# Kernel optimization log

Measured on AMD Instinct MI355X. Metric: run time of the kernel, lower is better.

Reference implementation:

```python
import jax, jax.numpy as jnp
import numpy as np

N = 50000          # total nodes
NPG = 100          # nodes per graph
G = N // NPG       # graphs
E_RAND = 800000    # random intra-graph edges (no self loops)
F_IN, HID, OUT, H, NCLS = 128, 64, 64, 2, 10
NEG_SLOPE = 0.2


def setup_inputs() -> dict:
    key = jax.random.key(0)
    ks = jax.random.split(key, 16)
    x = jax.random.normal(ks[0], (N, F_IN), dtype=jnp.float32)
    # intra-graph edges, guaranteed non-self; PyG GATConv then appends self loops
    g = jax.random.randint(ks[1], (E_RAND,), 0, G)
    dst_loc = jax.random.randint(ks[2], (E_RAND,), 0, NPG)
    off = jax.random.randint(ks[3], (E_RAND,), 1, NPG)  # 1..NPG-1 -> never self
    src_loc = (dst_loc + off) % NPG
    base = g * NPG
    src = jnp.concatenate([base + src_loc, jnp.arange(N)])  # + self loops
    dst = jnp.concatenate([base + dst_loc, jnp.arange(N)])
    edge_index = jnp.stack([src, dst]).astype(jnp.int64)
    batch = (jnp.arange(N) // NPG).astype(jnp.int64)  # sorted segment ids
    y = jax.random.randint(ks[4], (N,), 0, NCLS).astype(jnp.int64)
    s = 0.1
    params = dict(
        W1=jax.random.normal(ks[5], (F_IN, H * HID), jnp.float32) * s,
        a_src1=jax.random.normal(ks[6], (H, HID), jnp.float32) * s,
        a_dst1=jax.random.normal(ks[7], (H, HID), jnp.float32) * s,
        b1=jnp.zeros((HID,), jnp.float32),
        W2=jax.random.normal(ks[8], (HID, H * OUT), jnp.float32) * s,
        a_src2=jax.random.normal(ks[9], (H, OUT), jnp.float32) * s,
        a_dst2=jax.random.normal(ks[10], (H, OUT), jnp.float32) * s,
        b2=jnp.zeros((OUT,), jnp.float32),
        Wc=jax.random.normal(ks[11], (OUT, NCLS), jnp.float32) * s,
        bc=jnp.zeros((NCLS,), jnp.float32),
    )
    return dict(x=x, edge_index=edge_index, batch=batch, y=y, **params)


def gat_layer(x, W, a_src, a_dst, b, src, dst, n_nodes):
    # PyG GATConv, heads=H, concat=False: h = xW -> [N,H,C]
    h = (x @ W).reshape(n_nodes, a_src.shape[0], a_src.shape[1])
    al_s = jnp.sum(h * a_src[None], axis=-1)  # [N,H]
    al_d = jnp.sum(h * a_dst[None], axis=-1)  # [N,H]
    e = jax.nn.leaky_relu(al_s[src] + al_d[dst], NEG_SLOPE)  # [E,H]
    # segment softmax over incoming edges of each dst node
    m = jax.ops.segment_max(e, dst, num_segments=n_nodes)  # every node has a self loop
    p = jnp.exp(e - m[dst])
    z = jax.ops.segment_sum(p, dst, num_segments=n_nodes)
    alpha = p / z[dst]  # [E,H]
    out = jax.ops.segment_sum(alpha[:, :, None] * h[src], dst, num_segments=n_nodes)
    return out.mean(axis=1) + b  # concat=False -> head mean, then bias


def reference(x, edge_index, batch, y, W1, a_src1, a_dst1, b1,
              W2, a_src2, a_dst2, b2, Wc, bc):
    # Per-graph loop in the original is equivalent to one pass over the batched
    # graph: edges are intra-graph and batch is sorted, so concatenation of
    # per-graph outputs preserves node order.
    src, dst = edge_index[0], edge_index[1]
    n = x.shape[0]
    h = gat_layer(x, W1, a_src1, a_dst1, b1, src, dst, n)
    h = jax.nn.relu(h)
    h = gat_layer(h, W2, a_src2, a_dst2, b2, src, dst, n)
    preds = h @ Wc + bc  # [N, num_classes]
    return preds, y
```

## Files before the change

### kernel.cpp

```cpp
#include <hip/hip_runtime.h>
#include <math.h>


#define NPG 100
#define CAP 2560
#define EPB 4096

#define OFF_HT    0
#define OFF_R3    34816
#define OFF_SCNT  65280
#define OFF_SAS   71680
#define OFF_SAD   72704
#define OFF_SRZ   73728
#define OFF_SWC   74176
#define OFF_SBC   76736
#define SMEM_BYTES 76800

typedef __attribute__((ext_vector_type(8))) short bf16x8;
typedef __attribute__((ext_vector_type(4))) float f32x4;

__device__ __forceinline__ float lrelu(float x) { return x > 0.f ? x : 0.2f * x; }

__device__ __forceinline__ unsigned cvt_pk(float lo, float hi) {
    unsigned r;
    asm("v_cvt_pk_bf16_f32 %0, %1, %2" : "=v"(r) : "v"(lo), "v"(hi));
    return r;
}

__device__ __forceinline__ unsigned short f2bf(float f) {
    unsigned int u = __float_as_uint(f);
    return (unsigned short)((u + 0x7FFF + ((u >> 16) & 1)) >> 16);
}

__global__ __launch_bounds__(1024) void bucket2_kernel(const int* __restrict__ src,
                                                       const int* __restrict__ dst,
                                                       int* gcnt,
                                                       unsigned short* __restrict__ bucket,
                                                       int e) {
    __shared__ int hist[512];
    __shared__ int base[512];
    __shared__ unsigned int staged[EPB];
    int tid = threadIdx.x;
    int e0 = blockIdx.x * EPB;
    int cnt = min(EPB, e - e0);

    for (int i = tid; i < 512; i += 1024) hist[i] = 0;
    __syncthreads();

    for (int i = tid; i < cnt; i += 1024) {
        int d = dst[e0 + i];
        int s = src[e0 + i];
        int g = d / NPG;
        int dloc = d - g * NPG;
        int sloc = s - g * NPG;
        staged[i] = ((unsigned)g << 16) | ((unsigned)dloc << 8) | (unsigned)sloc;
        atomicAdd(&hist[g], 1);
    }
    __syncthreads();

    if (tid < 512) {
        int h = hist[tid];
        base[tid] = h ? atomicAdd(&gcnt[tid], h) : 0;
        hist[tid] = 0;
    }
    __syncthreads();

    for (int i = tid; i < cnt; i += 1024) {
        unsigned v = staged[i];
        int g = v >> 16;
        int pos = base[g] + atomicAdd(&hist[g], 1);
        if (pos < CAP)
            bucket[(size_t)g * CAP + pos] = (unsigned short)(v & 0xFFFFu);
    }
}

__global__ __launch_bounds__(256) void convert_w(const float* __restrict__ W1,
                                                 const float* __restrict__ W2,
                                                 unsigned short* __restrict__ W1T,
                                                 unsigned short* __restrict__ W2T,
                                                 int* gcnt, int G) {
    int stride = gridDim.x * 256;
    int t0 = blockIdx.x * 256 + threadIdx.x;
    for (int i = t0; i < 128 * 128; i += stride) {
        int k = i >> 7, c = i & 127;
        W1T[c * 128 + k] = f2bf(W1[i]);
    }
    for (int i = t0; i < 64 * 128; i += stride) {
        int k = i >> 7, c = i & 127;
        W2T[c * 64 + k] = f2bf(W2[i]);
    }
    for (int i = t0; i < G; i += stride) gcnt[i] = 0;
}

template <int K, int SA>
__device__ __forceinline__ void gemm_block(const unsigned short* sA,
                                           const unsigned short* __restrict__ WT,
                                           const float* __restrict__ a_src,
                                           const float* __restrict__ a_dst,
                                           unsigned short* sHT,
                                           float* sAs, float* sAd,
                                           int lane, int wave) {
    if (wave >= 14) return;
    int s = wave >> 1, h = wave & 1;
    int fr = lane & 15, fk = (lane >> 4) * 8;
    f32x4 acc[4];
#pragma unroll
    for (int t = 0; t < 4; ++t) acc[t] = (f32x4){0.f, 0.f, 0.f, 0.f};
#pragma unroll
    for (int ks = 0; ks < K / 32; ++ks) {
        bf16x8 a = *reinterpret_cast<const bf16x8*>(&sA[(s * 16 + fr) * SA + ks * 32 + fk]);
#pragma unroll
        for (int t = 0; t < 4; ++t) {
            bf16x8 b = *reinterpret_cast<const bf16x8*>(
                &WT[((h * 4 + t) * 16 + fr) * K + ks * 32 + fk]);
            acc[t] = __builtin_amdgcn_mfma_f32_16x16x32_bf16(a, b, acc[t], 0, 0, 0);
        }
    }
    int rb = s * 16 + (lane >> 4) * 4;
    float ps[4] = {0, 0, 0, 0}, pd[4] = {0, 0, 0, 0};
#pragma unroll
    for (int t = 0; t < 4; ++t) {
        int col = (h * 4 + t) * 16 + fr;
        float as_ = a_src[col], ad_ = a_dst[col];
        float v0 = acc[t][0], v1 = acc[t][1], v2 = acc[t][2], v3 = acc[t][3];
        ps[0] += v0 * as_; pd[0] += v0 * ad_;
        ps[1] += v1 * as_; pd[1] += v1 * ad_;
        ps[2] += v2 * as_; pd[2] += v2 * ad_;
        ps[3] += v3 * as_; pd[3] += v3 * ad_;
        *reinterpret_cast<uint2*>(&sHT[col * 136 + rb]) =
            make_uint2(cvt_pk(v0, v1), cvt_pk(v2, v3));
    }
#pragma unroll
    for (int off = 1; off <= 8; off <<= 1) {
#pragma unroll
        for (int j = 0; j < 4; ++j) {
            ps[j] += __shfl_xor(ps[j], off);
            pd[j] += __shfl_xor(pd[j], off);
        }
    }
    if (fr == 0) {
#pragma unroll
        for (int j = 0; j < 4; ++j) {
            int d = rb + j;
            sAs[d * 2 + h] = ps[j];
            sAd[d * 2 + h] = pd[j];
        }
    }
}

__device__ __forceinline__ void agg_heads(unsigned short* sP,
                                          const unsigned short* sHT,
                                          const unsigned* scnt,
                                          const float* sAs, const float* sAd,
                                          float* sRZ, f32x4 res[2],
                                          int lane, int wave) {
    for (int head = 0; head < 2; ++head) {
        for (int d = wave; d < NPG; d += 16) {
            float adh = sAd[d * 2 + head];
            unsigned w = scnt[d * 16 + (lane >> 2)];
            int sh = (lane & 3) * 8;
            unsigned m0 = (w >> sh) & 15u;
            unsigned m1 = (w >> (sh + 4)) & 15u;
            float4 a4 = *reinterpret_cast<const float4*>(&sAs[lane * 4]);
            float e0 = (head ? a4.y : a4.x) + adh;
            float e1 = (head ? a4.w : a4.z) + adh;
            float p0 = m0 ? (float)m0 * __expf(lrelu(e0)) : 0.f;
            float p1 = m1 ? (float)m1 * __expf(lrelu(e1)) : 0.f;
            float z = p0 + p1;
            for (int off = 32; off; off >>= 1) z += __shfl_xor(z, off);
            *reinterpret_cast<unsigned*>(&sP[d * 136 + lane * 2]) = cvt_pk(p0, p1);
            if (lane == 0) sRZ[d] = 1.f / z;
        }
        __syncthreads();
#pragma unroll
        for (int i = 0; i < 2; ++i) {
            int t = wave + 16 * i;
            if (t < 28) {
                int mt = t >> 2, nt = t & 3;
                int arow = mt * 16 + (lane & 15);
                int brow = head * 64 + nt * 16 + (lane & 15);
                int kofs = (lane >> 4) * 8;
                f32x4 acc = (f32x4){0.f, 0.f, 0.f, 0.f};
#pragma unroll
                for (int ks = 0; ks < 4; ++ks) {
                    bf16x8 a = *reinterpret_cast<const bf16x8*>(&sP[arow * 136 + ks * 32 + kofs]);
                    bf16x8 b = *reinterpret_cast<const bf16x8*>(&sHT[brow * 136 + ks * 32 + kofs]);
                    acc = __builtin_amdgcn_mfma_f32_16x16x32_bf16(a, b, acc, 0, 0, 0);
                }
                int dbase = mt * 16 + (lane >> 4) * 4;
#pragma unroll
                for (int r = 0; r < 4; ++r)
                    res[i][r] += acc[r] * sRZ[dbase + r];
            }
        }
        __syncthreads();
    }
}

__global__ __launch_bounds__(1024, 8) void graph_fused(
    const float* __restrict__ x,
    const unsigned short* __restrict__ W1T,
    const unsigned short* __restrict__ W2T,
    const float* __restrict__ as1, const float* __restrict__ ad1,
    const float* __restrict__ b1,
    const float* __restrict__ as2, const float* __restrict__ ad2,
    const float* __restrict__ b2,
    const float* __restrict__ Wc, const float* __restrict__ bc,
    const int* __restrict__ gcnt, const unsigned short* __restrict__ bucket,
    const int* __restrict__ y,
    float* __restrict__ preds, float* __restrict__ yout) {
    extern __shared__ char smem[];
    unsigned short* sHT  = (unsigned short*)(smem + OFF_HT);
    float*          sOut = (float*)(smem + OFF_HT);
    unsigned short* R3u  = (unsigned short*)(smem + OFF_R3);
    unsigned*       scnt = (unsigned*)(smem + OFF_SCNT);
    float*          sAs  = (float*)(smem + OFF_SAS);
    float*          sAd  = (float*)(smem + OFF_SAD);
    float*          sRZ  = (float*)(smem + OFF_SRZ);
    float*          sWc  = (float*)(smem + OFF_SWC);
    float*          sbc  = (float*)(smem + OFF_SBC);

    int g = blockIdx.x, gbase = g * NPG, tid = threadIdx.x;
    int lane = tid & 63, wave = tid >> 6;
    int cnt = min(gcnt[g], CAP);
    float4 z4 = make_float4(0.f, 0.f, 0.f, 0.f);

    for (int i = tid; i < 1600; i += 1024) scnt[i] = 0;
    for (int i = tid; i < 2176; i += 1024)
        *reinterpret_cast<float4*>((char*)sHT + i * 16) = z4;
    for (int i = tid; i < NPG * 16; i += 1024) {
        int r = i >> 4, kc = (i & 15) * 8;
        const float* xp = &x[(size_t)(gbase + r) * 128 + kc];
        float4 v0 = *reinterpret_cast<const float4*>(xp);
        float4 v1 = *reinterpret_cast<const float4*>(xp + 4);
        uint4 u = make_uint4(cvt_pk(v0.x, v0.y), cvt_pk(v0.z, v0.w),
                             cvt_pk(v1.x, v1.y), cvt_pk(v1.z, v1.w));
        *reinterpret_cast<uint4*>(&R3u[r * 136 + kc]) = u;
    }
    for (int i = tid; i < 12 * 17; i += 1024) {
        int r = 100 + i / 17, c = (i % 17) * 8;
        *reinterpret_cast<float4*>(&R3u[r * 136 + c]) = z4;
    }
    for (int i = tid; i < 640; i += 1024) sWc[i] = Wc[i];
    if (tid < 10) sbc[tid] = bc[tid];
    if (tid >= 32 && tid < 64) { sAs[192 + tid] = 0.f; sAd[192 + tid] = 0.f; }
    if (tid < NPG) yout[gbase + tid] = (float)y[gbase + tid];
    __syncthreads();
    for (int i = tid; i < cnt; i += 1024) {
        unsigned v = bucket[(size_t)g * CAP + i];
        atomicAdd(&scnt[(v >> 8) * 16 + ((v & 255) >> 3)], 1u << ((v & 7) * 4));
    }
    __syncthreads();

    gemm_block<128, 136>(R3u, W1T, as1, ad1, sHT, sAs, sAd, lane, wave);
    __syncthreads();

    f32x4 res[2];
    res[0] = (f32x4){0.f, 0.f, 0.f, 0.f};
    res[1] = (f32x4){0.f, 0.f, 0.f, 0.f};
    agg_heads(R3u, sHT, scnt, sAs, sAd, sRZ, res, lane, wave);

    {
        unsigned short* sB = R3u;
        int fr = lane & 15;
#pragma unroll
        for (int i = 0; i < 2; ++i) {
            int t = wave + 16 * i;
            if (t < 28) {
                int mt = t >> 2, nt = t & 3;
                int col = nt * 16 + fr;
                float bv = b1[col];
                int d0 = mt * 16 + (lane >> 4) * 4;
                unsigned u01 = cvt_pk(fmaxf(0.5f * res[i][0] + bv, 0.f),
                                      fmaxf(0.5f * res[i][1] + bv, 0.f));
                unsigned u23 = cvt_pk(fmaxf(0.5f * res[i][2] + bv, 0.f),
                                      fmaxf(0.5f * res[i][3] + bv, 0.f));
                if (d0 + 0 < NPG) sB[(d0 + 0) * 72 + col] = (unsigned short)u01;
                if (d0 + 1 < NPG) sB[(d0 + 1) * 72 + col] = (unsigned short)(u01 >> 16);
                if (d0 + 2 < NPG) sB[(d0 + 2) * 72 + col] = (unsigned short)u23;
                if (d0 + 3 < NPG) sB[(d0 + 3) * 72 + col] = (unsigned short)(u23 >> 16);
            }
        }
        for (int i = tid; i < 12 * 9; i += 1024) {
            int r = 100 + i / 9, c = (i % 9) * 8;
            *reinterpret_cast<float4*>(&sB[r * 72 + c]) = z4;
        }
    }
    __syncthreads();

    gemm_block<64, 72>(R3u, W2T, as2, ad2, sHT, sAs, sAd, lane, wave);
    __syncthreads();

    res[0] = (f32x4){0.f, 0.f, 0.f, 0.f};
    res[1] = (f32x4){0.f, 0.f, 0.f, 0.f};
    agg_heads(R3u, sHT, scnt, sAs, sAd, sRZ, res, lane, wave);

    {
        int fr = lane & 15;
#pragma unroll
        for (int i = 0; i < 2; ++i) {
            int t = wave + 16 * i;
            if (t < 28) {
                int mt = t >> 2, nt = t & 3;
                int col = nt * 16 + fr;
                float bv = b2[col];
#pragma unroll
                for (int r = 0; r < 4; ++r) {
                    int d = mt * 16 + (lane >> 4) * 4 + r;
                    if (d < NPG) sOut[d * 68 + col] = 0.5f * res[i][r] + bv;
                }
            }
        }
    }
    __syncthreads();

    for (int idx = tid; idx < NPG * 10; idx += 1024) {
        int d = idx / 10, j = idx % 10;
        float acc = sbc[j];
#pragma unroll
        for (int c = 0; c < 64; c += 4) {
            float4 h4 = *reinterpret_cast<const float4*>(&sOut[d * 68 + c]);
            acc += h4.x * sWc[(c + 0) * 10 + j];
            acc += h4.y * sWc[(c + 1) * 10 + j];
            acc += h4.z * sWc[(c + 2) * 10 + j];
            acc += h4.w * sWc[(c + 3) * 10 + j];
        }
        preds[(size_t)(gbase + d) * 10 + j] = acc;
    }
}

extern "C" void kernel_launch(void* const* d_in, const int* in_sizes, int n_in,
                              void* d_out, int out_size, void* d_ws, size_t ws_size,
                              hipStream_t stream) {
    const float* x   = (const float*)d_in[0];
    const int*   ei  = (const int*)d_in[1];
    const int*   y   = (const int*)d_in[3];
    const float* W1  = (const float*)d_in[4];
    const float* as1 = (const float*)d_in[5];
    const float* ad1 = (const float*)d_in[6];
    const float* b1  = (const float*)d_in[7];
    const float* W2  = (const float*)d_in[8];
    const float* as2 = (const float*)d_in[9];
    const float* ad2 = (const float*)d_in[10];
    const float* b2  = (const float*)d_in[11];
    const float* Wc  = (const float*)d_in[12];
    const float* bc  = (const float*)d_in[13];

    int n = in_sizes[0] / 128;
    int e = in_sizes[1] / 2;
    int G = n / NPG;
    const int* src = ei;
    const int* dst = ei + e;

    char* ws = (char*)d_ws;
    size_t off = 0;
    auto alloc = [&](size_t bytes) -> void* {
        void* p = ws + off;
        off = (off + bytes + 255) & ~size_t(255);
        return p;
    };
    unsigned short* W1T = (unsigned short*)alloc((size_t)128 * 128 * 2);
    unsigned short* W2T = (unsigned short*)alloc((size_t)128 * 64 * 2);
    int* gcnt = (int*)alloc((size_t)G * 4);
    unsigned short* bucket = (unsigned short*)alloc((size_t)G * CAP * 2);

    float* preds = (float*)d_out;
    float* yout  = preds + (size_t)n * 10;

    int bb = (e + EPB - 1) / EPB;

    convert_w<<<96, 256, 0, stream>>>(W1, W2, W1T, W2T, gcnt, G);
    bucket2_kernel<<<bb, 1024, 0, stream>>>(src, dst, gcnt, bucket, e);

    graph_fused<<<G, 1024, SMEM_BYTES, stream>>>(x, W1T, W2T, as1, ad1, b1,
                                                 as2, ad2, b2, Wc, bc,
                                                 gcnt, bucket, y, preds, yout);
}
```

Baseline: 78.82 us.

## Use MFMA for classifier head, prefetch GEMM operands, trim LDS zeroing

The final classifier matmul moves from a scalar per-thread loop over fp32 LDS to two bf16 MFMA ops per wave. Wc is pre-transposed to padded bf16 in the weight conversion kernel, and its LDS staging is removed. The layer GEMM now software-pipelines its A and B fragment loads one k-step ahead, the aggregation loop loads all fragments before issuing MFMAs, and LDS zeroing is limited to the padding columns. These changes cut LDS footprint and scalar FMA work at the cost of extra bf16 rounding in the classifier and higher register pressure.

```diff
diff --git a/kernel.cpp b/kernel.cpp
--- a/kernel.cpp
+++ b/kernel.cpp
@@ -12,9 +12,7 @@
 #define OFF_SAS   71680
 #define OFF_SAD   72704
 #define OFF_SRZ   73728
-#define OFF_SWC   74176
-#define OFF_SBC   76736
-#define SMEM_BYTES 76800
+#define SMEM_BYTES 74240
 
 typedef __attribute__((ext_vector_type(8))) short bf16x8;
 typedef __attribute__((ext_vector_type(4))) float f32x4;
@@ -76,8 +74,10 @@
 
 __global__ __launch_bounds__(256) void convert_w(const float* __restrict__ W1,
                                                  const float* __restrict__ W2,
+                                                 const float* __restrict__ Wc,
                                                  unsigned short* __restrict__ W1T,
                                                  unsigned short* __restrict__ W2T,
+                                                 unsigned short* __restrict__ WcT,
                                                  int* gcnt, int G) {
     int stride = gridDim.x * 256;
     int t0 = blockIdx.x * 256 + threadIdx.x;
@@ -88,6 +88,10 @@
     for (int i = t0; i < 64 * 128; i += stride) {
         int k = i >> 7, c = i & 127;
         W2T[c * 64 + k] = f2bf(W2[i]);
+    }
+    for (int i = t0; i < 16 * 64; i += stride) {
+        int j = i >> 6, k = i & 63;
+        WcT[i] = (j < 10) ? f2bf(Wc[k * 10 + j]) : (unsigned short)0;
     }
     for (int i = t0; i < G; i += stride) gcnt[i] = 0;
 }
@@ -103,19 +107,35 @@
     if (wave >= 14) return;
     int s = wave >> 1, h = wave & 1;
     int fr = lane & 15, fk = (lane >> 4) * 8;
+    const unsigned short* ap = sA + (s * 16 + fr) * SA + fk;
+    const unsigned short* bp = WT + (size_t)(h * 64 + fr) * K + fk;
     f32x4 acc[4];
 #pragma unroll
     for (int t = 0; t < 4; ++t) acc[t] = (f32x4){0.f, 0.f, 0.f, 0.f};
+
+    bf16x8 ac = *reinterpret_cast<const bf16x8*>(ap);
+    bf16x8 bc0 = *reinterpret_cast<const bf16x8*>(bp);
+    bf16x8 bc1 = *reinterpret_cast<const bf16x8*>(bp + 16 * K);
+    bf16x8 bc2 = *reinterpret_cast<const bf16x8*>(bp + 32 * K);
+    bf16x8 bc3 = *reinterpret_cast<const bf16x8*>(bp + 48 * K);
 #pragma unroll
     for (int ks = 0; ks < K / 32; ++ks) {
-        bf16x8 a = *reinterpret_cast<const bf16x8*>(&sA[(s * 16 + fr) * SA + ks * 32 + fk]);
-#pragma unroll
-        for (int t = 0; t < 4; ++t) {
-            bf16x8 b = *reinterpret_cast<const bf16x8*>(
-                &WT[((h * 4 + t) * 16 + fr) * K + ks * 32 + fk]);
-            acc[t] = __builtin_amdgcn_mfma_f32_16x16x32_bf16(a, b, acc[t], 0, 0, 0);
-        }
-    }
+        bf16x8 an = ac, bn0 = bc0, bn1 = bc1, bn2 = bc2, bn3 = bc3;
+        if (ks + 1 < K / 32) {
+            int o = (ks + 1) * 32;
+            an  = *reinterpret_cast<const bf16x8*>(ap + o);
+            bn0 = *reinterpret_cast<const bf16x8*>(bp + o);
+            bn1 = *reinterpret_cast<const bf16x8*>(bp + 16 * K + o);
+            bn2 = *reinterpret_cast<const bf16x8*>(bp + 32 * K + o);
+            bn3 = *reinterpret_cast<const bf16x8*>(bp + 48 * K + o);
+        }
+        acc[0] = __builtin_amdgcn_mfma_f32_16x16x32_bf16(ac, bc0, acc[0], 0, 0, 0);
+        acc[1] = __builtin_amdgcn_mfma_f32_16x16x32_bf16(ac, bc1, acc[1], 0, 0, 0);
+        acc[2] = __builtin_amdgcn_mfma_f32_16x16x32_bf16(ac, bc2, acc[2], 0, 0, 0);
+        acc[3] = __builtin_amdgcn_mfma_f32_16x16x32_bf16(ac, bc3, acc[3], 0, 0, 0);
+        ac = an; bc0 = bn0; bc1 = bn1; bc2 = bn2; bc3 = bn3;
+    }
+
     int rb = s * 16 + (lane >> 4) * 4;
     float ps[4] = {0, 0, 0, 0}, pd[4] = {0, 0, 0, 0};
 #pragma unroll
@@ -180,13 +200,16 @@
                 int arow = mt * 16 + (lane & 15);
                 int brow = head * 64 + nt * 16 + (lane & 15);
                 int kofs = (lane >> 4) * 8;
+                bf16x8 pa[4], hb[4];
+#pragma unroll
+                for (int ks = 0; ks < 4; ++ks) {
+                    pa[ks] = *reinterpret_cast<const bf16x8*>(&sP[arow * 136 + ks * 32 + kofs]);
+                    hb[ks] = *reinterpret_cast<const bf16x8*>(&sHT[brow * 136 + ks * 32 + kofs]);
+                }
                 f32x4 acc = (f32x4){0.f, 0.f, 0.f, 0.f};
 #pragma unroll
-                for (int ks = 0; ks < 4; ++ks) {
-                    bf16x8 a = *reinterpret_cast<const bf16x8*>(&sP[arow * 136 + ks * 32 + kofs]);
-                    bf16x8 b = *reinterpret_cast<const bf16x8*>(&sHT[brow * 136 + ks * 32 + kofs]);
-                    acc = __builtin_amdgcn_mfma_f32_16x16x32_bf16(a, b, acc, 0, 0, 0);
-                }
+                for (int ks = 0; ks < 4; ++ks)
+                    acc = __builtin_amdgcn_mfma_f32_16x16x32_bf16(pa[ks], hb[ks], acc, 0, 0, 0);
                 int dbase = mt * 16 + (lane >> 4) * 4;
 #pragma unroll
                 for (int r = 0; r < 4; ++r)
@@ -201,24 +224,23 @@
     const float* __restrict__ x,
     const unsigned short* __restrict__ W1T,
     const unsigned short* __restrict__ W2T,
+    const unsigned short* __restrict__ WcT,
     const float* __restrict__ as1, const float* __restrict__ ad1,
     const float* __restrict__ b1,
     const float* __restrict__ as2, const float* __restrict__ ad2,
     const float* __restrict__ b2,
-    const float* __restrict__ Wc, const float* __restrict__ bc,
+    const float* __restrict__ bc,
     const int* __restrict__ gcnt, const unsigned short* __restrict__ bucket,
     const int* __restrict__ y,
     float* __restrict__ preds, float* __restrict__ yout) {
     extern __shared__ char smem[];
     unsigned short* sHT  = (unsigned short*)(smem + OFF_HT);
-    float*          sOut = (float*)(smem + OFF_HT);
+    unsigned short* out2b = (unsigned short*)(smem + OFF_HT);
     unsigned short* R3u  = (unsigned short*)(smem + OFF_R3);
     unsigned*       scnt = (unsigned*)(smem + OFF_SCNT);
     float*          sAs  = (float*)(smem + OFF_SAS);
     float*          sAd  = (float*)(smem + OFF_SAD);
     float*          sRZ  = (float*)(smem + OFF_SRZ);
-    float*          sWc  = (float*)(smem + OFF_SWC);
-    float*          sbc  = (float*)(smem + OFF_SBC);
 
     int g = blockIdx.x, gbase = g * NPG, tid = threadIdx.x;
     int lane = tid & 63, wave = tid >> 6;
@@ -226,8 +248,10 @@
     float4 z4 = make_float4(0.f, 0.f, 0.f, 0.f);
 
     for (int i = tid; i < 1600; i += 1024) scnt[i] = 0;
-    for (int i = tid; i < 2176; i += 1024)
-        *reinterpret_cast<float4*>((char*)sHT + i * 16) = z4;
+    for (int i = tid; i < 256; i += 1024) {
+        int r = i >> 1, c = 112 + (i & 1) * 8;
+        *reinterpret_cast<float4*>(&sHT[r * 136 + c]) = z4;
+    }
     for (int i = tid; i < NPG * 16; i += 1024) {
         int r = i >> 4, kc = (i & 15) * 8;
         const float* xp = &x[(size_t)(gbase + r) * 128 + kc];
@@ -241,8 +265,6 @@
         int r = 100 + i / 17, c = (i % 17) * 8;
         *reinterpret_cast<float4*>(&R3u[r * 136 + c]) = z4;
     }
-    for (int i = tid; i < 640; i += 1024) sWc[i] = Wc[i];
-    if (tid < 10) sbc[tid] = bc[tid];
     if (tid >= 32 && tid < 64) { sAs[192 + tid] = 0.f; sAd[192 + tid] = 0.f; }
     if (tid < NPG) yout[gbase + tid] = (float)y[gbase + tid];
     __syncthreads();
@@ -304,28 +326,38 @@
                 int mt = t >> 2, nt = t & 3;
                 int col = nt * 16 + fr;
                 float bv = b2[col];
-#pragma unroll
-                for (int r = 0; r < 4; ++r) {
-                    int d = mt * 16 + (lane >> 4) * 4 + r;
-                    if (d < NPG) sOut[d * 68 + col] = 0.5f * res[i][r] + bv;
-                }
+                int d0 = mt * 16 + (lane >> 4) * 4;
+                unsigned u01 = cvt_pk(0.5f * res[i][0] + bv, 0.5f * res[i][1] + bv);
+                unsigned u23 = cvt_pk(0.5f * res[i][2] + bv, 0.5f * res[i][3] + bv);
+                out2b[(d0 + 0) * 72 + col] = (unsigned short)u01;
+                out2b[(d0 + 1) * 72 + col] = (unsigned short)(u01 >> 16);
+                out2b[(d0 + 2) * 72 + col] = (unsigned short)u23;
+                out2b[(d0 + 3) * 72 + col] = (unsigned short)(u23 >> 16);
             }
         }
     }
     __syncthreads();
 
-    for (int idx = tid; idx < NPG * 10; idx += 1024) {
-        int d = idx / 10, j = idx % 10;
-        float acc = sbc[j];
-#pragma unroll
-        for (int c = 0; c < 64; c += 4) {
-            float4 h4 = *reinterpret_cast<const float4*>(&sOut[d * 68 + c]);
-            acc += h4.x * sWc[(c + 0) * 10 + j];
-            acc += h4.y * sWc[(c + 1) * 10 + j];
-            acc += h4.z * sWc[(c + 2) * 10 + j];
-            acc += h4.w * sWc[(c + 3) * 10 + j];
-        }
-        preds[(size_t)(gbase + d) * 10 + j] = acc;
+    if (wave < 7) {
+        int fr = lane & 15, fk = (lane >> 4) * 8;
+        const unsigned short* ap = out2b + (wave * 16 + fr) * 72 + fk;
+        const unsigned short* bp = WcT + fr * 64 + fk;
+        bf16x8 a0 = *reinterpret_cast<const bf16x8*>(ap);
+        bf16x8 b0 = *reinterpret_cast<const bf16x8*>(bp);
+        bf16x8 a1 = *reinterpret_cast<const bf16x8*>(ap + 32);
+        bf16x8 b1 = *reinterpret_cast<const bf16x8*>(bp + 32);
+        f32x4 acc = (f32x4){0.f, 0.f, 0.f, 0.f};
+        acc = __builtin_amdgcn_mfma_f32_16x16x32_bf16(a0, b0, acc, 0, 0, 0);
+        acc = __builtin_amdgcn_mfma_f32_16x16x32_bf16(a1, b1, acc, 0, 0, 0);
+        if (fr < 10) {
+            float bcv = bc[fr];
+            int d0 = wave * 16 + (lane >> 4) * 4;
+#pragma unroll
+            for (int r = 0; r < 4; ++r) {
+                int d = d0 + r;
+                if (d < NPG) preds[(size_t)(gbase + d) * 10 + fr] = acc[r] + bcv;
+            }
+        }
     }
 }
 
@@ -361,6 +393,7 @@
     };
     unsigned short* W1T = (unsigned short*)alloc((size_t)128 * 128 * 2);
     unsigned short* W2T = (unsigned short*)alloc((size_t)128 * 64 * 2);
+    unsigned short* WcT = (unsigned short*)alloc((size_t)16 * 64 * 2);
     int* gcnt = (int*)alloc((size_t)G * 4);
     unsigned short* bucket = (unsigned short*)alloc((size_t)G * CAP * 2);
 
@@ -369,10 +402,10 @@
 
     int bb = (e + EPB - 1) / EPB;
 
-    convert_w<<<96, 256, 0, stream>>>(W1, W2, W1T, W2T, gcnt, G);
+    convert_w<<<96, 256, 0, stream>>>(W1, W2, Wc, W1T, W2T, WcT, gcnt, G);
     bucket2_kernel<<<bb, 1024, 0, stream>>>(src, dst, gcnt, bucket, e);
 
-    graph_fused<<<G, 1024, SMEM_BYTES, stream>>>(x, W1T, W2T, as1, ad1, b1,
-                                                 as2, ad2, b2, Wc, bc,
-                                                 gcnt, bucket, y, preds, yout);
-}
+    graph_fused<<<G, 1024, SMEM_BYTES, stream>>>(x, W1T, W2T, WcT,
+                                                 as1, ad1, b1, as2, ad2, b2,
+                                                 bc, gcnt, bucket, y, preds, yout);
+}
```

New measurement: 82.92 us. +5.2%, slower.
